# Kernel tuning notes

Hardware: AMD Instinct MI355X
Metric: run time of the kernel (lower is better)

## Reference

```python
import jax, jax.numpy as jnp
import numpy as np
from jax import lax


def setup_inputs() -> dict:
    key = jax.random.key(0)
    ks = jax.random.split(key, 8)
    B, S, H, L = 64, 512, 768, 9
    hidden = jax.random.normal(ks[0], (B, S, H), jnp.float32)
    label = jax.random.randint(ks[1], (B, S), 0, L, dtype=jnp.int32)
    mask = jnp.ones((B, S), jnp.int32)
    W = jax.random.normal(ks[2], (H, L), jnp.float32) * 0.02
    b = jnp.zeros((L,), jnp.float32)
    start_transitions = jax.random.normal(ks[3], (L,), jnp.float32) * 0.1
    end_transitions = jax.random.normal(ks[4], (L,), jnp.float32) * 0.1
    transitions = jax.random.normal(ks[5], (L, L), jnp.float32) * 0.1
    return dict(hidden=hidden, label=label, mask=mask, W=W, b=b,
                start_transitions=start_transitions,
                end_transitions=end_transitions,
                transitions=transitions)


def reference(hidden, label, mask, W, b, start_transitions, end_transitions, transitions):
    B, S, H = hidden.shape
    L = b.shape[0]
    # output_layer: [B,S,H] @ [H,L] -> emissions, then transpose to time-major [S,B,L]
    emissions = jnp.einsum('bsh,hl->bsl', hidden, W) + b
    em = jnp.transpose(emissions, (1, 0, 2))        # [S, B, L]
    tags = label.T                                   # [S, B]
    m = mask.T.astype(jnp.float32)                   # [S, B]

    def gather_tag(em_t, tag_t):
        # em_t [B,L], tag_t [B] -> [B]
        return jnp.take_along_axis(em_t, tag_t[:, None], axis=1)[:, 0]

    # ---- numerator: score of the gold path ----
    score0 = start_transitions[tags[0]] + gather_tag(em[0], tags[0])
    def num_step(carry, x):
        score, prev = carry
        em_t, tag_t, m_t = x
        s = transitions[prev, tag_t] + gather_tag(em_t, tag_t)
        score = score + s * m_t
        prev = jnp.where(m_t > 0, tag_t, prev)
        return (score, prev), None
    (score, last_gold), _ = lax.scan(num_step, (score0, tags[0]), (em[1:], tags[1:], m[1:]))
    score = score + end_transitions[last_gold]

    # ---- denominator: forward algorithm (logsumexp DP) ----
    alpha0 = start_transitions[None, :] + em[0]      # [B, L]
    def fwd_step(alpha, x):
        em_t, m_t = x
        nxt = jax.nn.logsumexp(alpha[:, :, None] + transitions[None, :, :] + em_t[:, None, :], axis=1)
        alpha = jnp.where(m_t[:, None] > 0, nxt, alpha)
        return alpha, None
    alphaT, _ = lax.scan(fwd_step, alpha0, (em[1:], m[1:]))
    logZ = jax.nn.logsumexp(alphaT + end_transitions[None, :], axis=1)

    llh = jnp.sum(score - logZ)                      # reduction='sum'
    loss = -llh / B

    # ---- Viterbi decode (decode() is called without mask -> full length) ----
    v0 = start_transitions[None, :] + em[0]
    def vit_step(v, em_t):
        scores = v[:, :, None] + transitions[None, :, :] + em_t[:, None, :]  # [B, L, L]
        return jnp.max(scores, axis=1), jnp.argmax(scores, axis=1)
    vT, hist = lax.scan(vit_step, v0, em[1:])        # hist [S-1, B, L]
    last_tag = jnp.argmax(vT + end_transitions[None, :], axis=1)  # [B]
    def back_step(tag, bp_t):
        prev = jnp.take_along_axis(bp_t, tag[:, None], axis=1)[:, 0]
        return prev, prev
    _, prevs = lax.scan(back_step, last_tag, hist, reverse=True)  # [S-1, B]
    path = jnp.concatenate([prevs, last_tag[None, :]], axis=0).T  # [B, S]

    # ---- accuracy bookkeeping (label > 0 mask) ----
    label_flat = label.reshape(-1)
    label_mask = (label_flat > 0).astype(jnp.int32)
    predict = path.reshape(-1).astype(jnp.int32) * label_mask
    correct = jnp.sum((predict == label_flat).astype(jnp.float32))
    return loss, correct, predict, label_flat
```

## Files before the change

kernel.cpp:

```cpp
#include <hip/hip_runtime.h>
#include <hip/hip_bf16.h>

#define NB 64
#define NS 512
#define NH 768
#define NL 9
#define NROWS (NB*NS)
#define EMN (NROWS*NL)

__device__ __forceinline__ float readlane_f(float v, int l) {
    return __int_as_float(__builtin_amdgcn_readlane(__float_as_int(v), l));
}
__device__ __forceinline__ unsigned long long readlane_u64(unsigned long long v, int l) {
    unsigned int lo = (unsigned int)__builtin_amdgcn_readlane((int)(unsigned int)(v & 0xffffffffULL), l);
    unsigned int hi = (unsigned int)__builtin_amdgcn_readlane((int)(unsigned int)(v >> 32), l);
    return ((unsigned long long)hi << 32) | (unsigned long long)lo;
}

__global__ __launch_bounds__(256) void k_gemm(const float* __restrict__ hidden,
                                              const float* __restrict__ W,
                                              const float* __restrict__ bias,
                                              float* __restrict__ em,
                                              float* __restrict__ out) {
    int tid = threadIdx.x;
    int lane = tid & 63;
    int w = blockIdx.x * 4 + (tid >> 6);
    if (blockIdx.x == 0 && tid == 0) { out[0] = 0.f; out[1] = 0.f; }

    float4 Wr[3][9];
    const float4* Wp = (const float4*)W;
#pragma unroll
    for (int c = 0; c < 3; c++) {
        const float4* p = Wp + 9 * lane + 576 * c;
#pragma unroll
        for (int q = 0; q < 9; q++) Wr[c][q] = p[q];
    }
    float bz[NL];
#pragma unroll
    for (int j = 0; j < NL; j++) bz[j] = bias[j];

#pragma unroll
    for (int r = 0; r < 4; r++) {
        int row = 4 * w + r;
        const float* hp = hidden + (size_t)row * NH;
        float4 h[3];
#pragma unroll
        for (int c = 0; c < 3; c++) h[c] = *(const float4*)(hp + 4 * lane + 256 * c);
        float acc[NL];
#pragma unroll
        for (int j = 0; j < NL; j++) acc[j] = 0.f;
#pragma unroll
        for (int c = 0; c < 3; c++) {
            const float hv[4] = { h[c].x, h[c].y, h[c].z, h[c].w };
#pragma unroll
            for (int kk = 0; kk < 4; kk++) {
#pragma unroll
                for (int j = 0; j < NL; j++) {
                    int fl = kk * 9 + j;
                    const float4& wq = Wr[c][fl >> 2];
                    float wv = (fl & 3) == 0 ? wq.x : (fl & 3) == 1 ? wq.y : (fl & 3) == 2 ? wq.z : wq.w;
                    acc[j] = fmaf(hv[kk], wv, acc[j]);
                }
            }
        }
#pragma unroll
        for (int m = 1; m < 64; m <<= 1) {
#pragma unroll
            for (int j = 0; j < NL; j++) acc[j] += __shfl_xor(acc[j], m);
        }
        if (lane == 0) {
            float* o = em + (size_t)row * NL;
#pragma unroll
            for (int j = 0; j < NL; j++) o[j] = acc[j] + bz[j];
        }
    }
}

__global__ __launch_bounds__(256) void k_dp(const float* __restrict__ em,
                                            const int* __restrict__ label,
                                            const int* __restrict__ mask,
                                            const float* __restrict__ startT,
                                            const float* __restrict__ endT,
                                            const float* __restrict__ trans,
                                            float* __restrict__ logZ,
                                            float* __restrict__ score,
                                            unsigned char* __restrict__ path) {
    __shared__ float s_em[NS * NL];
    __shared__ float s_v[NS * NL];
    __shared__ unsigned char s_bp[NS * NL];
    __shared__ int s_mk[NS];
    __shared__ float s_T[NL * NL];

    int bx = blockIdx.x;
    int tid = threadIdx.x;
    int role = bx >> 6;
    int b = bx & 63;

    {
        const float4* ef = (const float4*)(em + (size_t)b * NS * NL);
        float4* sf = (float4*)s_em;
        for (int q = tid; q < NS * NL / 4; q += 256) sf[q] = ef[q];
        if (tid < NS / 4) ((int4*)s_mk)[tid] = ((const int4*)(mask + b * NS))[tid];
        if (tid < NL * NL) s_T[tid] = trans[tid];
    }
    __syncthreads();

    if (role == 0) {
        if (tid < 64) {
            int j9 = tid < NL ? tid : NL - 1;
            float Mcol[NL];
#pragma unroll
            for (int i = 0; i < NL; i++) Mcol[i] = __expf(s_T[i * NL + j9]);
            float a = __expf(startT[j9] + s_em[j9]);
            int eacc = 0;
            float epre[4]; int mpre[4];
#pragma unroll
            for (int p = 0; p < 4; p++) { epre[p] = s_em[(1 + p) * NL + j9]; mpre[p] = s_mk[1 + p]; }
#pragma unroll 4
            for (int t = 1; t < NS; ++t) {
                float emv = epre[0]; int mv = mpre[0];
                epre[0] = epre[1]; epre[1] = epre[2]; epre[2] = epre[3];
                mpre[0] = mpre[1]; mpre[1] = mpre[2]; mpre[2] = mpre[3];
                int tn = t + 4; tn = tn < NS ? tn : NS - 1;
                epre[3] = s_em[tn * NL + j9]; mpre[3] = s_mk[tn];
                float p0 = readlane_f(a, 0) * Mcol[0];
                float p1 = readlane_f(a, 1) * Mcol[1];
                float p2 = readlane_f(a, 2) * Mcol[2];
                float p3 = readlane_f(a, 3) * Mcol[3];
                float p4 = readlane_f(a, 4) * Mcol[4];
                float p5 = readlane_f(a, 5) * Mcol[5];
                float p6 = readlane_f(a, 6) * Mcol[6];
                float p7 = readlane_f(a, 7) * Mcol[7];
                float p8 = readlane_f(a, 8) * Mcol[8];
                float s = (((p0 + p1) + (p2 + p3)) + ((p4 + p5) + (p6 + p7))) + p8;
                float anew = __expf(emv) * s;
                a = (mv > 0) ? anew : a;
                if ((t & 7) == 0) {
                    float c0 = readlane_f(a, 0), c1 = readlane_f(a, 1), c2 = readlane_f(a, 2);
                    float c3 = readlane_f(a, 3), c4 = readlane_f(a, 4), c5 = readlane_f(a, 5);
                    float c6 = readlane_f(a, 6), c7 = readlane_f(a, 7), c8 = readlane_f(a, 8);
                    float c = (((c0 + c1) + (c2 + c3)) + ((c4 + c5) + (c6 + c7))) + c8;
                    int ex = ((__float_as_int(c) >> 23) & 255) - 127;
                    a = ldexpf(a, -ex);
                    eacc += ex;
                }
            }
            float z = a * __expf(endT[j9]);
            float c0 = readlane_f(z, 0), c1 = readlane_f(z, 1), c2 = readlane_f(z, 2);
            float c3 = readlane_f(z, 3), c4 = readlane_f(z, 4), c5 = readlane_f(z, 5);
            float c6 = readlane_f(z, 6), c7 = readlane_f(z, 7), c8 = readlane_f(z, 8);
            float c = (((c0 + c1) + (c2 + c3)) + ((c4 + c5) + (c6 + c7))) + c8;
            if (tid == 0) logZ[b] = (float)eacc * 0.6931471805599453f + __logf(c);
        }
    } else if (role == 1) {
        if (tid < 64) {
            int j9 = tid < NL ? tid : NL - 1;
            float Tcol[NL];
#pragma unroll
            for (int i = 0; i < NL; i++) Tcol[i] = s_T[i * NL + j9];
            float v = startT[j9] + s_em[j9];
            if (tid < NL) { s_v[tid] = v; s_bp[tid] = (unsigned char)tid; }
            float epre[4];
#pragma unroll
            for (int p = 0; p < 4; p++) epre[p] = s_em[(1 + p) * NL + j9];
#pragma unroll 4
            for (int t = 1; t < NS; ++t) {
                float emv = epre[0];
                epre[0] = epre[1]; epre[1] = epre[2]; epre[2] = epre[3];
                int tn = t + 4; tn = tn < NS ? tn : NS - 1;
                epre[3] = s_em[tn * NL + j9];
                float m0 = readlane_f(v, 0) + Tcol[0];
                float m1 = readlane_f(v, 1) + Tcol[1];
                float m2 = readlane_f(v, 2) + Tcol[2];
                float m3 = readlane_f(v, 3) + Tcol[3];
                float m4 = readlane_f(v, 4) + Tcol[4];
                float m5 = readlane_f(v, 5) + Tcol[5];
                float m6 = readlane_f(v, 6) + Tcol[6];
                float m7 = readlane_f(v, 7) + Tcol[7];
                float m8 = readlane_f(v, 8) + Tcol[8];
                float M = fmaxf(fmaxf(fmaxf(fmaxf(m0, m1), fmaxf(m2, m3)),
                                      fmaxf(fmaxf(m4, m5), fmaxf(m6, m7))), m8);
                v = M + emv;
                if (tid < NL) s_v[t * NL + tid] = v;
            }
        }
        __syncthreads();
#pragma unroll
        for (int rep = 0; rep < 2; rep++) {
            int t = 1 + tid + 256 * rep;
            if (t < NS) {
                float vp[NL], emt[NL];
#pragma unroll
                for (int i = 0; i < NL; i++) vp[i] = s_v[(t - 1) * NL + i];
#pragma unroll
                for (int j = 0; j < NL; j++) emt[j] = s_em[t * NL + j];
#pragma unroll
                for (int j = 0; j < NL; j++) {
                    float e = emt[j];
                    float val[NL];
#pragma unroll
                    for (int i = 0; i < NL; i++) val[i] = (vp[i] + s_T[i * NL + j]) + e;
                    bool c01 = val[0] >= val[1]; float m01 = c01 ? val[0] : val[1]; int i01 = c01 ? 0 : 1;
                    bool c23 = val[2] >= val[3]; float m23 = c23 ? val[2] : val[3]; int i23 = c23 ? 2 : 3;
                    bool c45 = val[4] >= val[5]; float m45 = c45 ? val[4] : val[5]; int i45 = c45 ? 4 : 5;
                    bool c67 = val[6] >= val[7]; float m67 = c67 ? val[6] : val[7]; int i67 = c67 ? 6 : 7;
                    bool ca = m01 >= m23; float ma = ca ? m01 : m23; int ia = ca ? i01 : i23;
                    bool cb = m45 >= m67; float mb = cb ? m45 : m67; int ib = cb ? i45 : i67;
                    bool cc = ma >= mb;  float mc = cc ? ma : mb;  int ic = cc ? ia : ib;
                    bool cd = mc >= val[8]; int bi = cd ? ic : 8;
                    s_bp[t * NL + j] = (unsigned char)bi;
                }
            }
        }
        __syncthreads();
        if (tid < 64) {
            int lane = tid;
            float bb = s_v[(NS - 1) * NL + 0] + endT[0]; int lt = 0;
#pragma unroll
            for (int jj = 1; jj < NL; jj++) {
                float fj = s_v[(NS - 1) * NL + jj] + endT[jj];
                if (fj > bb) { bb = fj; lt = jj; }
            }
            unsigned long long G[8];
#pragma unroll
            for (int r = 0; r < 8; r++) {
                int t0 = (lane * 8 + r) * NL;
                unsigned long long g = 0;
#pragma unroll
                for (int x = 0; x < NL; x++) g |= (unsigned long long)s_bp[t0 + x] << (4 * x);
                G[r] = g;
            }
            unsigned long long A = 0x876543210ULL;
#pragma unroll
            for (int r = 7; r >= 0; r--) {
                unsigned long long An = 0;
#pragma unroll
                for (int x = 0; x < NL; x++) {
                    int ax = (int)((A >> (4 * x)) & 15ULL);
                    int gv = (int)((G[r] >> (4 * ax)) & 15ULL);
                    An |= (unsigned long long)gv << (4 * x);
                }
                A = An;
            }
            int e = 0; int cur = lt;
            for (int ll = 63; ll >= 0; --ll) {
                if (lane == ll) e = cur;
                unsigned long long Al = readlane_u64(A, ll);
                cur = (int)((Al >> (4 * cur)) & 15ULL);
            }
            unsigned long long pw = 0; int c2 = e;
#pragma unroll
            for (int r = 7; r >= 0; r--) {
                pw |= (unsigned long long)c2 << (8 * r);
                c2 = (int)((G[r] >> (4 * c2)) & 15ULL);
            }
            *(unsigned long long*)(path + (size_t)b * NS + lane * 8) = pw;
        }
    } else {
        if (tid < 64) {
            int lane = tid;
            const int* lb = label + b * NS;
            int t0 = lane * 8;
            int lab[8]; int mk[8];
#pragma unroll
            for (int r = 0; r < 8; r++) { lab[r] = lb[t0 + r]; mk[r] = s_mk[t0 + r]; }
            if (lane == 0) mk[0] = 1;
            int h = 0, sl = 0;
#pragma unroll
            for (int r = 0; r < 8; r++) { if (mk[r] > 0) { h = 1; sl = lab[r]; } }
#pragma unroll
            for (int d = 1; d < 64; d <<= 1) {
                int ho = __shfl_up(h, d);
                int so = __shfl_up(sl, d);
                if (!h) { h = ho; sl = so; }
            }
            int lg = __shfl(sl, 63);
            int incoming = __shfl_up(sl, 1);
            float sc = 0.f;
            int prevr = (lane == 0) ? lab[0] : incoming;
#pragma unroll
            for (int r = 0; r < 8; r++) {
                int t = t0 + r;
                if (t > 0) {
                    float s = s_T[prevr * NL + lab[r]] + s_em[t * NL + lab[r]];
                    sc += s * (float)mk[r];
                }
                if (mk[r] > 0) prevr = lab[r];
            }
            if (lane == 0) {
                int g0 = lab[0];
                sc += startT[g0] + s_em[g0] + endT[lg];
            }
#pragma unroll
            for (int d = 1; d < 64; d <<= 1) sc += __shfl_xor(sc, d);
            if (lane == 0) score[b] = sc;
        }
    }
}

__global__ __launch_bounds__(256) void k_fin(const int* __restrict__ label,
                                             const unsigned char* __restrict__ path,
                                             const float* __restrict__ logZ,
                                             const float* __restrict__ score,
                                             float* __restrict__ out) {
    int b = blockIdx.x;
    int tid = threadIdx.x;
    float cnt = 0.f;
#pragma unroll
    for (int q = 0; q < 2; q++) {
        int t = tid + q * 256;
        int idx = b * NS + t;
        int lab = label[idx];
        int p = (int)path[idx];
        int pred = (lab > 0) ? p : 0;
        out[2 + idx] = (float)pred;
        out[2 + NROWS + idx] = (float)lab;
        cnt += (pred == lab) ? 1.f : 0.f;
    }
#pragma unroll
    for (int d = 1; d < 64; d <<= 1) cnt += __shfl_xor(cnt, d);
    if ((tid & 63) == 0) atomicAdd(out + 1, cnt);
    if (b == 0 && tid < 64) {
        float dsc = score[tid] - logZ[tid];
#pragma unroll
        for (int d = 1; d < 64; d <<= 1) dsc += __shfl_xor(dsc, d);
        if (tid == 0) out[0] = -dsc / (float)NB;
    }
}

extern "C" void kernel_launch(void* const* d_in, const int* in_sizes, int n_in,
                              void* d_out, int out_size, void* d_ws, size_t ws_size,
                              hipStream_t stream) {
    const float* hidden = (const float*)d_in[0];
    const int*   label  = (const int*)d_in[1];
    const int*   mask   = (const int*)d_in[2];
    const float* W      = (const float*)d_in[3];
    const float* bias   = (const float*)d_in[4];
    const float* startT = (const float*)d_in[5];
    const float* endT   = (const float*)d_in[6];
    const float* trans  = (const float*)d_in[7];
    float* out = (float*)d_out;

    float* ws     = (float*)d_ws;
    float* em     = ws;
    float* logZv  = ws + EMN;
    float* scorev = ws + EMN + 64;
    unsigned char* path = (unsigned char*)(ws + EMN + 128);

    k_gemm<<<2048, 256, 0, stream>>>(hidden, W, bias, em, out);
    k_dp<<<192, 256, 0, stream>>>(em, label, mask, startT, endT, trans, logZv, scorev, path);
    k_fin<<<64, 256, 0, stream>>>(label, path, logZv, scorev, out);
}
```

Measured before the change: 219.0 us.

## Fuse finalize into DP kernel, merge gold-score role, use DPP reductions

Removes the k_fin launch by writing predictions, labels and the correct count straight from the Viterbi blocks and accumulating the loss with atomics. The gold-path score moves into a second wave of the forward-algorithm blocks, cutting the DP grid from 192 to 128 blocks. The GEMM's cross-lane shuffle reduction becomes DPP row and broadcast adds with the result taken from lane 63. The exp of the emissions is hoisted into the prefetch stage, off the recurrence critical path. Atomic float accumulation of the loss makes the summation order nondeterministic.

```diff
diff --git a/kernel.cpp b/kernel.cpp
--- a/kernel.cpp
+++ b/kernel.cpp
@@ -15,6 +15,20 @@
     unsigned int lo = (unsigned int)__builtin_amdgcn_readlane((int)(unsigned int)(v & 0xffffffffULL), l);
     unsigned int hi = (unsigned int)__builtin_amdgcn_readlane((int)(unsigned int)(v >> 32), l);
     return ((unsigned long long)hi << 32) | (unsigned long long)lo;
+}
+template <int CTRL>
+__device__ __forceinline__ float dpp_add(float x) {
+    int t = __builtin_amdgcn_update_dpp(0, __float_as_int(x), CTRL, 0xf, 0xf, false);
+    return x + __int_as_float(t);
+}
+__device__ __forceinline__ float wave_sum_to63(float x) {
+    x = dpp_add<0x111>(x);
+    x = dpp_add<0x112>(x);
+    x = dpp_add<0x114>(x);
+    x = dpp_add<0x118>(x);
+    x = dpp_add<0x142>(x);
+    x = dpp_add<0x143>(x);
+    return x;
 }
 
 __global__ __launch_bounds__(256) void k_gemm(const float* __restrict__ hidden,
@@ -63,15 +77,13 @@
                 }
             }
         }
-#pragma unroll
-        for (int m = 1; m < 64; m <<= 1) {
-#pragma unroll
-            for (int j = 0; j < NL; j++) acc[j] += __shfl_xor(acc[j], m);
-        }
-        if (lane == 0) {
+        float s[NL];
+#pragma unroll
+        for (int j = 0; j < NL; j++) s[j] = wave_sum_to63(acc[j]);
+        if (lane == 63) {
             float* o = em + (size_t)row * NL;
 #pragma unroll
-            for (int j = 0; j < NL; j++) o[j] = acc[j] + bz[j];
+            for (int j = 0; j < NL; j++) o[j] = s[j] + bz[j];
         }
     }
 }
@@ -82,18 +94,16 @@
                                             const float* __restrict__ startT,
                                             const float* __restrict__ endT,
                                             const float* __restrict__ trans,
-                                            float* __restrict__ logZ,
-                                            float* __restrict__ score,
-                                            unsigned char* __restrict__ path) {
+                                            float* __restrict__ out) {
     __shared__ float s_em[NS * NL];
     __shared__ float s_v[NS * NL];
     __shared__ unsigned char s_bp[NS * NL];
+    __shared__ unsigned char s_path[NS];
     __shared__ int s_mk[NS];
     __shared__ float s_T[NL * NL];
 
     int bx = blockIdx.x;
     int tid = threadIdx.x;
-    int role = bx >> 6;
     int b = bx & 63;
 
     {
@@ -105,7 +115,7 @@
     }
     __syncthreads();
 
-    if (role == 0) {
+    if (bx < NB) {
         if (tid < 64) {
             int j9 = tid < NL ? tid : NL - 1;
             float Mcol[NL];
@@ -113,16 +123,16 @@
             for (int i = 0; i < NL; i++) Mcol[i] = __expf(s_T[i * NL + j9]);
             float a = __expf(startT[j9] + s_em[j9]);
             int eacc = 0;
-            float epre[4]; int mpre[4];
-#pragma unroll
-            for (int p = 0; p < 4; p++) { epre[p] = s_em[(1 + p) * NL + j9]; mpre[p] = s_mk[1 + p]; }
+            float xpre[4]; int mpre[4];
+#pragma unroll
+            for (int p = 0; p < 4; p++) { xpre[p] = __expf(s_em[(1 + p) * NL + j9]); mpre[p] = s_mk[1 + p]; }
 #pragma unroll 4
             for (int t = 1; t < NS; ++t) {
-                float emv = epre[0]; int mv = mpre[0];
-                epre[0] = epre[1]; epre[1] = epre[2]; epre[2] = epre[3];
+                float xev = xpre[0]; int mv = mpre[0];
+                xpre[0] = xpre[1]; xpre[1] = xpre[2]; xpre[2] = xpre[3];
                 mpre[0] = mpre[1]; mpre[1] = mpre[2]; mpre[2] = mpre[3];
                 int tn = t + 4; tn = tn < NS ? tn : NS - 1;
-                epre[3] = s_em[tn * NL + j9]; mpre[3] = s_mk[tn];
+                xpre[3] = __expf(s_em[tn * NL + j9]); mpre[3] = s_mk[tn];
                 float p0 = readlane_f(a, 0) * Mcol[0];
                 float p1 = readlane_f(a, 1) * Mcol[1];
                 float p2 = readlane_f(a, 2) * Mcol[2];
@@ -133,7 +143,7 @@
                 float p7 = readlane_f(a, 7) * Mcol[7];
                 float p8 = readlane_f(a, 8) * Mcol[8];
                 float s = (((p0 + p1) + (p2 + p3)) + ((p4 + p5) + (p6 + p7))) + p8;
-                float anew = __expf(emv) * s;
+                float anew = xev * s;
                 a = (mv > 0) ? anew : a;
                 if ((t & 7) == 0) {
                     float c0 = readlane_f(a, 0), c1 = readlane_f(a, 1), c2 = readlane_f(a, 2);
@@ -150,16 +160,56 @@
             float c3 = readlane_f(z, 3), c4 = readlane_f(z, 4), c5 = readlane_f(z, 5);
             float c6 = readlane_f(z, 6), c7 = readlane_f(z, 7), c8 = readlane_f(z, 8);
             float c = (((c0 + c1) + (c2 + c3)) + ((c4 + c5) + (c6 + c7))) + c8;
-            if (tid == 0) logZ[b] = (float)eacc * 0.6931471805599453f + __logf(c);
-        }
-    } else if (role == 1) {
+            if (tid == 0) {
+                float lz = (float)eacc * 0.6931471805599453f + __logf(c);
+                atomicAdd(out, lz * (1.0f / (float)NB));
+            }
+        } else if (tid < 128) {
+            int lane = tid & 63;
+            const int* lb = label + b * NS;
+            int t0 = lane * 8;
+            int lab[8]; int mk[8];
+#pragma unroll
+            for (int r = 0; r < 8; r++) { lab[r] = lb[t0 + r]; mk[r] = s_mk[t0 + r]; }
+            if (lane == 0) mk[0] = 1;
+            int h = 0, sl = 0;
+#pragma unroll
+            for (int r = 0; r < 8; r++) { if (mk[r] > 0) { h = 1; sl = lab[r]; } }
+#pragma unroll
+            for (int d = 1; d < 64; d <<= 1) {
+                int ho = __shfl_up(h, d);
+                int so = __shfl_up(sl, d);
+                if (!h) { h = ho; sl = so; }
+            }
+            int lg = __shfl(sl, 63);
+            int incoming = __shfl_up(sl, 1);
+            float sc = 0.f;
+            int prevr = (lane == 0) ? lab[0] : incoming;
+#pragma unroll
+            for (int r = 0; r < 8; r++) {
+                int t = t0 + r;
+                if (t > 0) {
+                    float s = s_T[prevr * NL + lab[r]] + s_em[t * NL + lab[r]];
+                    sc += s * (float)mk[r];
+                }
+                if (mk[r] > 0) prevr = lab[r];
+            }
+            if (lane == 0) {
+                int g0 = lab[0];
+                sc += startT[g0] + s_em[g0] + endT[lg];
+            }
+#pragma unroll
+            for (int d = 1; d < 64; d <<= 1) sc += __shfl_xor(sc, d);
+            if (lane == 0) atomicAdd(out, -sc * (1.0f / (float)NB));
+        }
+    } else {
         if (tid < 64) {
             int j9 = tid < NL ? tid : NL - 1;
             float Tcol[NL];
 #pragma unroll
             for (int i = 0; i < NL; i++) Tcol[i] = s_T[i * NL + j9];
             float v = startT[j9] + s_em[j9];
-            if (tid < NL) { s_v[tid] = v; s_bp[tid] = (unsigned char)tid; }
+            if (tid < NL) s_v[tid] = v;
             float epre[4];
 #pragma unroll
             for (int p = 0; p < 4; p++) epre[p] = s_em[(1 + p) * NL + j9];
@@ -210,6 +260,8 @@
                     bool cd = mc >= val[8]; int bi = cd ? ic : 8;
                     s_bp[t * NL + j] = (unsigned char)bi;
                 }
+            } else if (t == NS) {
+                s_bp[0 * NL + tid - 255] = 0;
             }
         }
         __syncthreads();
@@ -226,8 +278,12 @@
             for (int r = 0; r < 8; r++) {
                 int t0 = (lane * 8 + r) * NL;
                 unsigned long long g = 0;
-#pragma unroll
-                for (int x = 0; x < NL; x++) g |= (unsigned long long)s_bp[t0 + x] << (4 * x);
+                if (lane == 0 && r == 0) {
+                    g = 0x876543210ULL;
+                } else {
+#pragma unroll
+                    for (int x = 0; x < NL; x++) g |= (unsigned long long)s_bp[t0 + x] << (4 * x);
+                }
                 G[r] = g;
             }
             unsigned long long A = 0x876543210ULL;
@@ -254,77 +310,25 @@
                 pw |= (unsigned long long)c2 << (8 * r);
                 c2 = (int)((G[r] >> (4 * c2)) & 15ULL);
             }
-            *(unsigned long long*)(path + (size_t)b * NS + lane * 8) = pw;
-        }
-    } else {
-        if (tid < 64) {
-            int lane = tid;
-            const int* lb = label + b * NS;
-            int t0 = lane * 8;
-            int lab[8]; int mk[8];
-#pragma unroll
-            for (int r = 0; r < 8; r++) { lab[r] = lb[t0 + r]; mk[r] = s_mk[t0 + r]; }
-            if (lane == 0) mk[0] = 1;
-            int h = 0, sl = 0;
-#pragma unroll
-            for (int r = 0; r < 8; r++) { if (mk[r] > 0) { h = 1; sl = lab[r]; } }
-#pragma unroll
-            for (int d = 1; d < 64; d <<= 1) {
-                int ho = __shfl_up(h, d);
-                int so = __shfl_up(sl, d);
-                if (!h) { h = ho; sl = so; }
-            }
-            int lg = __shfl(sl, 63);
-            int incoming = __shfl_up(sl, 1);
-            float sc = 0.f;
-            int prevr = (lane == 0) ? lab[0] : incoming;
-#pragma unroll
-            for (int r = 0; r < 8; r++) {
-                int t = t0 + r;
-                if (t > 0) {
-                    float s = s_T[prevr * NL + lab[r]] + s_em[t * NL + lab[r]];
-                    sc += s * (float)mk[r];
-                }
-                if (mk[r] > 0) prevr = lab[r];
-            }
-            if (lane == 0) {
-                int g0 = lab[0];
-                sc += startT[g0] + s_em[g0] + endT[lg];
-            }
-#pragma unroll
-            for (int d = 1; d < 64; d <<= 1) sc += __shfl_xor(sc, d);
-            if (lane == 0) score[b] = sc;
-        }
-    }
-}
-
-__global__ __launch_bounds__(256) void k_fin(const int* __restrict__ label,
-                                             const unsigned char* __restrict__ path,
-                                             const float* __restrict__ logZ,
-                                             const float* __restrict__ score,
-                                             float* __restrict__ out) {
-    int b = blockIdx.x;
-    int tid = threadIdx.x;
-    float cnt = 0.f;
-#pragma unroll
-    for (int q = 0; q < 2; q++) {
-        int t = tid + q * 256;
-        int idx = b * NS + t;
-        int lab = label[idx];
-        int p = (int)path[idx];
-        int pred = (lab > 0) ? p : 0;
-        out[2 + idx] = (float)pred;
-        out[2 + NROWS + idx] = (float)lab;
-        cnt += (pred == lab) ? 1.f : 0.f;
-    }
-#pragma unroll
-    for (int d = 1; d < 64; d <<= 1) cnt += __shfl_xor(cnt, d);
-    if ((tid & 63) == 0) atomicAdd(out + 1, cnt);
-    if (b == 0 && tid < 64) {
-        float dsc = score[tid] - logZ[tid];
-#pragma unroll
-        for (int d = 1; d < 64; d <<= 1) dsc += __shfl_xor(dsc, d);
-        if (tid == 0) out[0] = -dsc / (float)NB;
+            *(unsigned long long*)(s_path + lane * 8) = pw;
+        }
+        __syncthreads();
+        const int* lb = label + b * NS;
+        float cnt = 0.f;
+#pragma unroll
+        for (int q = 0; q < 2; q++) {
+            int t = tid + q * 256;
+            int idx = b * NS + t;
+            int lab = lb[t];
+            int p = (int)s_path[t];
+            int pred = (lab > 0) ? p : 0;
+            out[2 + idx] = (float)pred;
+            out[2 + NROWS + idx] = (float)lab;
+            cnt += (pred == lab) ? 1.f : 0.f;
+        }
+#pragma unroll
+        for (int d = 1; d < 64; d <<= 1) cnt += __shfl_xor(cnt, d);
+        if ((tid & 63) == 0) atomicAdd(out + 1, cnt);
     }
 }
 
@@ -341,13 +345,8 @@
     const float* trans  = (const float*)d_in[7];
     float* out = (float*)d_out;
 
-    float* ws     = (float*)d_ws;
-    float* em     = ws;
-    float* logZv  = ws + EMN;
-    float* scorev = ws + EMN + 64;
-    unsigned char* path = (unsigned char*)(ws + EMN + 128);
+    float* em = (float*)d_ws;
 
     k_gemm<<<2048, 256, 0, stream>>>(hidden, W, bias, em, out);
-    k_dp<<<192, 256, 0, stream>>>(em, label, mask, startT, endT, trans, logZv, scorev, path);
-    k_fin<<<64, 256, 0, stream>>>(label, path, logZv, scorev, out);
-}
+    k_dp<<<128, 256, 0, stream>>>(em, label, mask, startT, endT, trans, out);
+}
```

Result: no change. 216.9 us (-1.0%).
